# Optimization experiments

Hardware: AMD Instinct MI355X
Metric: run time of the kernel (lower is better)

Reference implementation:

```python
import jax, jax.numpy as jnp
import numpy as np

NEG_INF = jnp.finfo(jnp.float32).min


def _continual_mask(attach_test_after, Q, K, test_num, chunk_size):
    """Boolean allowed-mask [B, 1, Q, K] replicating get_continual_mask +
    the per-batch test-query/train-key override in forward()."""
    k_train = K - test_num * chunk_size
    q_train = Q - test_num * chunk_size
    qi = jnp.arange(Q)[:, None]          # [Q,1]
    kj = jnp.arange(K)[None, :]          # [1,K]
    # base causal mask with diagonal offset K-Q (train queries)
    base = kj <= qi + (K - Q)            # [Q,K]
    # block-diagonal tril for test-query / test-key region
    dq = qi - q_train                    # local test row (negative for train rows, unused there)
    dk = kj - k_train
    block = (kj >= k_train) & (dk <= dq) & ((dk // chunk_size) == (dq // chunk_size))
    # per-batch: test query in chunk n may see train keys <= attach_test_after[b, n]
    chunk_idx = jnp.clip(dq[:, 0], 0, None) // chunk_size          # [Q]
    att = attach_test_after[:, chunk_idx]                          # [B,Q]
    train_key_allowed = kj[None, :, :] <= att[:, :, None]          # [B,Q,K]
    allowed = jnp.where(qi < q_train, base[None],
                        jnp.where(kj[None] < k_train, train_key_allowed, block[None]))
    return allowed[:, None]              # [B,1,Q,K]


def setup_inputs() -> dict:
    key = jax.random.key(0)
    k1, k2, k3, k4 = jax.random.split(key, 4)
    B, L, H, D = 4, 2048, 8, 64
    test_num, train_len = 64, 1536
    return {
        "queries": jax.random.normal(k1, (B, L, H, D), dtype=jnp.float32),
        "keys": jax.random.normal(k2, (B, L, H, D), dtype=jnp.float32),
        "values": jax.random.normal(k3, (B, L, H, D), dtype=jnp.float32),
        "attach_test_after": jax.random.randint(k4, (B, test_num), 0, train_len).astype(jnp.int64),
        "train_len": train_len,
    }


def reference(queries, keys, values, attach_test_after, train_len):
    B, Lq, H, Dqk = queries.shape
    test_num = attach_test_after.shape[1]
    chunk_size = (Lq - train_len) // test_num
    q = jnp.transpose(queries, (0, 2, 1, 3))   # [B,H,Lq,D]
    k = jnp.transpose(keys, (0, 2, 1, 3))      # [B,H,Lk,D]
    v = jnp.transpose(values, (0, 2, 1, 3))    # [B,H,Lk,Dv]
    Lk = k.shape[2]
    # vanilla path: scaled QK^T + continual mask + softmax + AV
    logits = jnp.einsum('bhmd,bhnd->bhmn', q, k) / jnp.sqrt(jnp.float32(Dqk))
    allowed = _continual_mask(attach_test_after, Lq, Lk, test_num, chunk_size)
    logits = jnp.where(allowed, logits, NEG_INF)
    attn = jax.nn.softmax(logits, axis=-1)
    out = jnp.einsum('bhmn,bhnd->bhmd', attn, v)
    return out.transpose(0, 2, 1, 3).reshape(B, Lq, H * v.shape[-1])  # b l (h d)
```

## Files before the change

kernel.cpp:

```cpp
#include <hip/hip_runtime.h>
#include <hip/hip_bf16.h>

typedef __bf16 bf16_t;
typedef __bf16 bf16x8 __attribute__((ext_vector_type(8)));
typedef float  f32x4  __attribute__((ext_vector_type(4)));

#define MFMA16(a, b, c) __builtin_amdgcn_mfma_f32_16x16x32_bf16((a), (b), (c), 0, 0, 0)

constexpr int Bc = 4, Lc = 2048, Hc = 8, Dc = 64;
constexpr int HD = Hc * Dc;
constexpr int TRAINc = 1536;
constexpr int KT = 64;
constexpr int PST = 64;
constexpr float QSCALE = 0.125f * 1.4426950408889634f;

__global__ void prep_k(const float* __restrict__ K, bf16_t* __restrict__ Kb) {
  size_t g = ((size_t)blockIdx.x * 256 + threadIdx.x) * 8;
  float4 a = *(const float4*)(K + g);
  float4 b = *(const float4*)(K + g + 4);
  bf16x8 v;
  v[0] = (bf16_t)a.x; v[1] = (bf16_t)a.y; v[2] = (bf16_t)a.z; v[3] = (bf16_t)a.w;
  v[4] = (bf16_t)b.x; v[5] = (bf16_t)b.y; v[6] = (bf16_t)b.z; v[7] = (bf16_t)b.w;
  *(bf16x8*)(Kb + g) = v;
}

__global__ void prep_v(const float* __restrict__ V, bf16_t* __restrict__ Vt) {
  __shared__ bf16_t T[64][72];
  const int bid = blockIdx.x;
  const int kt = bid & 31, h = (bid >> 5) & 7, b = bid >> 8;
  const int t = (int)threadIdx.x;
  {
    int kl = t >> 2, dp = (t & 3) << 4;
    const float* s = V + ((size_t)(b * Lc + kt * 64 + kl) * Hc + h) * Dc + dp;
    bf16x8 v0, v1;
    float4 f;
    f = *(const float4*)(s);      v0[0]=(bf16_t)f.x; v0[1]=(bf16_t)f.y; v0[2]=(bf16_t)f.z; v0[3]=(bf16_t)f.w;
    f = *(const float4*)(s + 4);  v0[4]=(bf16_t)f.x; v0[5]=(bf16_t)f.y; v0[6]=(bf16_t)f.z; v0[7]=(bf16_t)f.w;
    f = *(const float4*)(s + 8);  v1[0]=(bf16_t)f.x; v1[1]=(bf16_t)f.y; v1[2]=(bf16_t)f.z; v1[3]=(bf16_t)f.w;
    f = *(const float4*)(s + 12); v1[4]=(bf16_t)f.x; v1[5]=(bf16_t)f.y; v1[6]=(bf16_t)f.z; v1[7]=(bf16_t)f.w;
    *(bf16x8*)&T[kl][dp] = v0;
    *(bf16x8*)&T[kl][dp + 8] = v1;
  }
  __syncthreads();
  {
    int d = t >> 2, kp = (t & 3) << 4;
    bf16x8 o0, o1;
#pragma unroll
    for (int i = 0; i < 8; ++i) { o0[i] = T[kp + i][d]; o1[i] = T[kp + 8 + i][d]; }
    bf16_t* dst = Vt + ((size_t)((b * Hc + h) * Dc + d)) * Lc + kt * 64 + kp;
    *(bf16x8*)dst = o0;
    *(bf16x8*)(dst + 8) = o1;
  }
}

static __device__ __forceinline__ void load16(const bf16_t* g, bf16_t* l) {
  __builtin_amdgcn_global_load_lds(
      (const __attribute__((address_space(1))) unsigned int*)g,
      (__attribute__((address_space(3))) unsigned int*)l, 16, 0, 0);
}

__global__ __launch_bounds__(256, 4)
void continual_attn(const float* __restrict__ Qg, const bf16_t* __restrict__ Kb,
                    const bf16_t* __restrict__ Vt, const int* __restrict__ ATT,
                    float* __restrict__ OUT)
{
  __shared__ __align__(16) bf16_t Klds[2][KT * 64];
  __shared__ __align__(16) bf16_t Vlds[2][Dc * KT];
  __shared__ __align__(16) bf16_t Plds[4][16 * PST];

  const int bid  = blockIdx.x;
  const int qblk = 31 - (bid >> 5);
  const int h    = bid & 7;
  const int b    = (bid >> 3) & 3;
  const int q0   = qblk * 64;

  const int tid  = (int)threadIdx.x;
  const int wave = tid >> 6;
  const int lane = tid & 63;
  const int quad = lane >> 4;
  const int col  = lane & 15;
  const int qw   = q0 + wave * 16;

  const bool testblk = (q0 >= TRAINc);
  int kend[4], cstart[4], qir[4];
#pragma unroll
  for (int r = 0; r < 4; ++r) {
    int qi = qw + quad * 4 + r;
    qir[r] = qi;
    if (testblk) {
      kend[r]   = ATT[b * 64 + ((qi - TRAINc) >> 3)] + 1;
      cstart[r] = qi & ~7;
    } else {
      kend[r]   = qi + 1;
      cstart[r] = 0;
    }
  }

  int ntA, ndiag, kfull_end;
  if (testblk) {
    int c0 = (q0 - TRAINc) >> 3;
    int amax = 0;
#pragma unroll
    for (int i = 0; i < 8; ++i) {
      int a = ATT[b * 64 + c0 + i];
      amax = (a > amax) ? a : amax;
    }
    int w0 = (qw - TRAINc) >> 3;
    int a0 = ATT[b * 64 + w0], a1 = ATT[b * 64 + w0 + 1];
    kfull_end = ((a0 < a1) ? a0 : a1) + 1;
    ntA = (amax >> 6) + 1;
    ndiag = 1;
  } else {
    ntA = qblk + 1;
    ndiag = 0;
    kfull_end = qw + 1;
  }
  const int ntot = ntA + ndiag;

  const size_t bhQ = (size_t)b * Lc * HD + (size_t)h * Dc;

  const int kr = tid >> 3;
  const bf16_t* ksrcA = Kb + bhQ + (size_t)kr * HD + (((tid & 7) ^ (kr & 7)) << 3);
  const bf16_t* vsrcA = Vt + ((size_t)((b * Hc + h) * Dc + kr)) * Lc + (((tid & 7) ^ (kr & 7)) << 3);
  const bf16_t* vsrcB = vsrcA + (size_t)32 * Lc;

  bf16x8 aq[2];
  {
    const float* qp = Qg + bhQ + (size_t)(qw + col) * HD + quad * 8;
#pragma unroll
    for (int t = 0; t < 2; ++t) {
      float4 lo = *(const float4*)(qp + t * 32);
      float4 hi = *(const float4*)(qp + t * 32 + 4);
      bf16x8 v;
      v[0] = (bf16_t)(lo.x * QSCALE); v[1] = (bf16_t)(lo.y * QSCALE);
      v[2] = (bf16_t)(lo.z * QSCALE); v[3] = (bf16_t)(lo.w * QSCALE);
      v[4] = (bf16_t)(hi.x * QSCALE); v[5] = (bf16_t)(hi.y * QSCALE);
      v[6] = (bf16_t)(hi.z * QSCALE); v[7] = (bf16_t)(hi.w * QSCALE);
      aq[t] = v;
    }
  }

  float lsumL[4] = {0.f, 0.f, 0.f, 0.f};
  f32x4 o[4] = {{0,0,0,0},{0,0,0,0},{0,0,0,0},{0,0,0,0}};
  const int cA = ((quad ^ (col & 7)) << 3);

  load16(ksrcA, Klds[0] + wave * 512);
  load16(ksrcA + (size_t)32 * HD, Klds[0] + 2048 + wave * 512);
  load16(vsrcA, Vlds[0] + wave * 512);
  load16(vsrcB, Vlds[0] + 2048 + wave * 512);

  for (int ti = 0; ti < ntot; ++ti) {
    const int buf = ti & 1;
    __syncthreads();

    if (ti + 1 < ntot) {
      const int kn = (ti + 1 < ntA) ? (ti + 1) * KT : q0;
      load16(ksrcA + (size_t)kn * HD, Klds[1 - buf] + wave * 512);
      load16(ksrcA + (size_t)(kn + 32) * HD, Klds[1 - buf] + 2048 + wave * 512);
      load16(vsrcA + kn, Vlds[1 - buf] + wave * 512);
      load16(vsrcB + kn, Vlds[1 - buf] + 2048 + wave * 512);
    }

    const bf16_t* kb = Klds[buf];
    const bf16_t* vbuf = Vlds[buf];
    const int k0 = (ti < ntA) ? ti * KT : q0;

    f32x4 sf[4] = {{0,0,0,0},{0,0,0,0},{0,0,0,0},{0,0,0,0}};
#pragma unroll
    for (int kg = 0; kg < 4; ++kg) {
      const bf16_t* krow = kb + (kg * 16 + col) * 64;
      bf16x8 k0f = *(const bf16x8*)(krow + cA);
      bf16x8 k1f = *(const bf16x8*)(krow + (cA ^ 32));
      sf[kg] = MFMA16(aq[0], k0f, sf[kg]);
      sf[kg] = MFMA16(aq[1], k1f, sf[kg]);
    }

    const int mode = (ti >= ntA) ? 2 : ((k0 + KT <= kfull_end) ? 0 : 1);
    if (mode == 1) {
#pragma unroll
      for (int kg = 0; kg < 4; ++kg) {
        const int kgv = k0 + kg * 16 + col;
#pragma unroll
        for (int r = 0; r < 4; ++r)
          if (kgv >= kend[r]) sf[kg][r] = -1e30f;
      }
    } else if (mode == 2) {
#pragma unroll
      for (int kg = 0; kg < 4; ++kg) {
        const int kgv = k0 + kg * 16 + col;
#pragma unroll
        for (int r = 0; r < 4; ++r)
          if (kgv < cstart[r] || kgv > qir[r]) sf[kg][r] = -1e30f;
      }
    }

    bf16_t* pw = Plds[wave];
#pragma unroll
    for (int kg = 0; kg < 4; ++kg) {
#pragma unroll
      for (int r = 0; r < 4; ++r) {
        float p = __builtin_amdgcn_exp2f(sf[kg][r]);
        lsumL[r] += p;
        const int row = quad * 4 + r;
        pw[row * PST + (((kg * 2 + (col >> 3)) ^ (row & 7)) << 3) + (col & 7)] = (bf16_t)p;
      }
    }
    bf16x8 pa0 = *(const bf16x8*)&pw[col * PST + cA];
    bf16x8 pa1 = *(const bf16x8*)&pw[col * PST + (cA ^ 32)];

#pragma unroll
    for (int t = 0; t < 4; ++t) {
      const bf16_t* vrow = vbuf + (t * 16 + col) * 64;
      bf16x8 v0 = *(const bf16x8*)(vrow + cA);
      bf16x8 v1 = *(const bf16x8*)(vrow + (cA ^ 32));
      o[t] = MFMA16(pa0, v0, o[t]);
      o[t] = MFMA16(pa1, v1, o[t]);
    }
  }

#pragma unroll
  for (int r = 0; r < 4; ++r) {
    float rs = lsumL[r];
    rs += __shfl_xor(rs, 1);
    rs += __shfl_xor(rs, 2);
    rs += __shfl_xor(rs, 4);
    rs += __shfl_xor(rs, 8);
    float inv = 1.f / rs;
    int qi = qw + quad * 4 + r;
    float* op = OUT + ((size_t)b * Lc + qi) * HD + (size_t)h * Dc + col;
    op[0]  = o[0][r] * inv;
    op[16] = o[1][r] * inv;
    op[32] = o[2][r] * inv;
    op[48] = o[3][r] * inv;
  }
}

extern "C" void kernel_launch(void* const* d_in, const int* in_sizes, int n_in,
                              void* d_out, int out_size, void* d_ws, size_t ws_size,
                              hipStream_t stream) {
  const float* Q   = (const float*)d_in[0];
  const float* K   = (const float*)d_in[1];
  const float* V   = (const float*)d_in[2];
  const int*   ATT = (const int*)d_in[3];
  float* OUT = (float*)d_out;
  (void)in_sizes; (void)n_in; (void)out_size; (void)ws_size;

  const size_t NE = (size_t)Bc * Lc * Hc * Dc;
  bf16_t* Kb = (bf16_t*)d_ws;
  bf16_t* Vt = Kb + NE;

  prep_k<<<dim3((unsigned)(NE / 8 / 256)), dim3(256), 0, stream>>>(K, Kb);
  prep_v<<<dim3(Bc * Hc * (Lc / 64)), dim3(256), 0, stream>>>(V, Vt);
  continual_attn<<<dim3(Bc * Hc * 32), dim3(256), 0, stream>>>(Q, Kb, Vt, ATT, OUT);
}
```

Baseline: 131.6 us.

## Use two-wave blocks with 32 query rows per wave and merge K/V prep kernels

The attention kernel moves from 4 waves handling 16 query rows each to 2 waves handling 32 rows each. Every K and V fragment read from LDS now feeds MFMAs for two row blocks, which halves LDS traffic per unit of compute. The K and V conversion kernels are also merged into a single launch to save one kernel launch. In exchange each wave needs more registers, and each block has fewer waves to hide latency, with a launch bound of 2 blocks per SIMD group.

```diff
diff --git a/kernel.cpp b/kernel.cpp
--- a/kernel.cpp
+++ b/kernel.cpp
@@ -10,25 +10,25 @@
 constexpr int Bc = 4, Lc = 2048, Hc = 8, Dc = 64;
 constexpr int HD = Hc * Dc;
 constexpr int TRAINc = 1536;
-constexpr int KT = 64;
-constexpr int PST = 64;
 constexpr float QSCALE = 0.125f * 1.4426950408889634f;
 
-__global__ void prep_k(const float* __restrict__ K, bf16_t* __restrict__ Kb) {
-  size_t g = ((size_t)blockIdx.x * 256 + threadIdx.x) * 8;
-  float4 a = *(const float4*)(K + g);
-  float4 b = *(const float4*)(K + g + 4);
-  bf16x8 v;
-  v[0] = (bf16_t)a.x; v[1] = (bf16_t)a.y; v[2] = (bf16_t)a.z; v[3] = (bf16_t)a.w;
-  v[4] = (bf16_t)b.x; v[5] = (bf16_t)b.y; v[6] = (bf16_t)b.z; v[7] = (bf16_t)b.w;
-  *(bf16x8*)(Kb + g) = v;
-}
-
-__global__ void prep_v(const float* __restrict__ V, bf16_t* __restrict__ Vt) {
+__global__ void prep_kv(const float* __restrict__ K, const float* __restrict__ V,
+                        bf16_t* __restrict__ Kb, bf16_t* __restrict__ Vt) {
   __shared__ bf16_t T[64][72];
-  const int bid = blockIdx.x;
+  const int bid0 = blockIdx.x;
+  const int t = (int)threadIdx.x;
+  if (bid0 < 2048) {
+    size_t g = ((size_t)bid0 * 256 + t) * 8;
+    float4 a = *(const float4*)(K + g);
+    float4 b = *(const float4*)(K + g + 4);
+    bf16x8 v;
+    v[0] = (bf16_t)a.x; v[1] = (bf16_t)a.y; v[2] = (bf16_t)a.z; v[3] = (bf16_t)a.w;
+    v[4] = (bf16_t)b.x; v[5] = (bf16_t)b.y; v[6] = (bf16_t)b.z; v[7] = (bf16_t)b.w;
+    *(bf16x8*)(Kb + g) = v;
+    return;
+  }
+  const int bid = bid0 - 2048;
   const int kt = bid & 31, h = (bid >> 5) & 7, b = bid >> 8;
-  const int t = (int)threadIdx.x;
   {
     int kl = t >> 2, dp = (t & 3) << 4;
     const float* s = V + ((size_t)(b * Lc + kt * 64 + kl) * Hc + h) * Dc + dp;
@@ -59,14 +59,14 @@
       (__attribute__((address_space(3))) unsigned int*)l, 16, 0, 0);
 }
 
-__global__ __launch_bounds__(256, 4)
+__global__ __launch_bounds__(128, 2)
 void continual_attn(const float* __restrict__ Qg, const bf16_t* __restrict__ Kb,
                     const bf16_t* __restrict__ Vt, const int* __restrict__ ATT,
                     float* __restrict__ OUT)
 {
-  __shared__ __align__(16) bf16_t Klds[2][KT * 64];
-  __shared__ __align__(16) bf16_t Vlds[2][Dc * KT];
-  __shared__ __align__(16) bf16_t Plds[4][16 * PST];
+  __shared__ __align__(16) bf16_t Klds[2][64 * 64];
+  __shared__ __align__(16) bf16_t Vlds[2][64 * 64];
+  __shared__ __align__(16) bf16_t Plds[2][32 * 64];
 
   const int bid  = blockIdx.x;
   const int qblk = 31 - (bid >> 5);
@@ -79,24 +79,27 @@
   const int lane = tid & 63;
   const int quad = lane >> 4;
   const int col  = lane & 15;
-  const int qw   = q0 + wave * 16;
+  const int qw   = q0 + wave * 32;
 
   const bool testblk = (q0 >= TRAINc);
-  int kend[4], cstart[4], qir[4];
-#pragma unroll
-  for (int r = 0; r < 4; ++r) {
-    int qi = qw + quad * 4 + r;
-    qir[r] = qi;
-    if (testblk) {
-      kend[r]   = ATT[b * 64 + ((qi - TRAINc) >> 3)] + 1;
-      cstart[r] = qi & ~7;
-    } else {
-      kend[r]   = qi + 1;
-      cstart[r] = 0;
-    }
-  }
-
-  int ntA, ndiag, kfull_end;
+  int kend[2][4], cstart[2][4], qir[2][4];
+#pragma unroll
+  for (int rb = 0; rb < 2; ++rb) {
+#pragma unroll
+    for (int r = 0; r < 4; ++r) {
+      int qi = qw + rb * 16 + quad * 4 + r;
+      qir[rb][r] = qi;
+      if (testblk) {
+        kend[rb][r]   = ATT[b * 64 + ((qi - TRAINc) >> 3)] + 1;
+        cstart[rb][r] = qi & ~7;
+      } else {
+        kend[rb][r]   = qi + 1;
+        cstart[rb][r] = 0;
+      }
+    }
+  }
+
+  int ntA, ntot, kfull_end;
   if (testblk) {
     int c0 = (q0 - TRAINc) >> 3;
     int amax = 0;
@@ -106,27 +109,32 @@
       amax = (a > amax) ? a : amax;
     }
     int w0 = (qw - TRAINc) >> 3;
-    int a0 = ATT[b * 64 + w0], a1 = ATT[b * 64 + w0 + 1];
-    kfull_end = ((a0 < a1) ? a0 : a1) + 1;
+    int amin = 0x7fffffff;
+#pragma unroll
+    for (int i = 0; i < 4; ++i) {
+      int a = ATT[b * 64 + w0 + i];
+      amin = (a < amin) ? a : amin;
+    }
+    kfull_end = amin + 1;
     ntA = (amax >> 6) + 1;
-    ndiag = 1;
+    ntot = ntA + 1;
   } else {
     ntA = qblk + 1;
-    ndiag = 0;
+    ntot = ntA;
     kfull_end = qw + 1;
   }
-  const int ntot = ntA + ndiag;
 
   const size_t bhQ = (size_t)b * Lc * HD + (size_t)h * Dc;
 
   const int kr = tid >> 3;
-  const bf16_t* ksrcA = Kb + bhQ + (size_t)kr * HD + (((tid & 7) ^ (kr & 7)) << 3);
-  const bf16_t* vsrcA = Vt + ((size_t)((b * Hc + h) * Dc + kr)) * Lc + (((tid & 7) ^ (kr & 7)) << 3);
-  const bf16_t* vsrcB = vsrcA + (size_t)32 * Lc;
-
-  bf16x8 aq[2];
-  {
-    const float* qp = Qg + bhQ + (size_t)(qw + col) * HD + quad * 8;
+  const int sl = ((tid & 7) ^ (kr & 7)) << 3;
+  const bf16_t* ksrc0 = Kb + bhQ + (size_t)kr * HD + sl;
+  const bf16_t* vsrc0 = Vt + ((size_t)((b * Hc + h) * Dc + kr)) * Lc + sl;
+
+  bf16x8 aq[2][2];
+#pragma unroll
+  for (int rb = 0; rb < 2; ++rb) {
+    const float* qp = Qg + bhQ + (size_t)(qw + rb * 16 + col) * HD + quad * 8;
 #pragma unroll
     for (int t = 0; t < 2; ++t) {
       float4 lo = *(const float4*)(qp + t * 32);
@@ -136,102 +144,126 @@
       v[2] = (bf16_t)(lo.z * QSCALE); v[3] = (bf16_t)(lo.w * QSCALE);
       v[4] = (bf16_t)(hi.x * QSCALE); v[5] = (bf16_t)(hi.y * QSCALE);
       v[6] = (bf16_t)(hi.z * QSCALE); v[7] = (bf16_t)(hi.w * QSCALE);
-      aq[t] = v;
-    }
-  }
-
-  float lsumL[4] = {0.f, 0.f, 0.f, 0.f};
-  f32x4 o[4] = {{0,0,0,0},{0,0,0,0},{0,0,0,0},{0,0,0,0}};
+      aq[rb][t] = v;
+    }
+  }
+
+  float lsumL[2][4] = {{0.f,0.f,0.f,0.f},{0.f,0.f,0.f,0.f}};
+  f32x4 o[2][4] = {};
   const int cA = ((quad ^ (col & 7)) << 3);
 
-  load16(ksrcA, Klds[0] + wave * 512);
-  load16(ksrcA + (size_t)32 * HD, Klds[0] + 2048 + wave * 512);
-  load16(vsrcA, Vlds[0] + wave * 512);
-  load16(vsrcB, Vlds[0] + 2048 + wave * 512);
+#pragma unroll
+  for (int c = 0; c < 4; ++c) {
+    load16(ksrc0 + (size_t)(16 * c) * HD, Klds[0] + wave * 512 + c * 1024);
+    load16(vsrc0 + (size_t)(16 * c) * Lc, Vlds[0] + wave * 512 + c * 1024);
+  }
 
   for (int ti = 0; ti < ntot; ++ti) {
     const int buf = ti & 1;
     __syncthreads();
 
     if (ti + 1 < ntot) {
-      const int kn = (ti + 1 < ntA) ? (ti + 1) * KT : q0;
-      load16(ksrcA + (size_t)kn * HD, Klds[1 - buf] + wave * 512);
-      load16(ksrcA + (size_t)(kn + 32) * HD, Klds[1 - buf] + 2048 + wave * 512);
-      load16(vsrcA + kn, Vlds[1 - buf] + wave * 512);
-      load16(vsrcB + kn, Vlds[1 - buf] + 2048 + wave * 512);
+      const int kn = (ti + 1 < ntA) ? (ti + 1) * 64 : q0;
+      bf16_t* kd = Klds[1 - buf] + wave * 512;
+      bf16_t* vd = Vlds[1 - buf] + wave * 512;
+#pragma unroll
+      for (int c = 0; c < 4; ++c) {
+        load16(ksrc0 + (size_t)(kn + 16 * c) * HD, kd + c * 1024);
+        load16(vsrc0 + (size_t)(16 * c) * Lc + kn, vd + c * 1024);
+      }
     }
 
     const bf16_t* kb = Klds[buf];
-    const bf16_t* vbuf = Vlds[buf];
-    const int k0 = (ti < ntA) ? ti * KT : q0;
-
-    f32x4 sf[4] = {{0,0,0,0},{0,0,0,0},{0,0,0,0},{0,0,0,0}};
+    const bf16_t* vb = Vlds[buf];
+    const int k0 = (ti < ntA) ? ti * 64 : q0;
+
+    f32x4 sf[2][4] = {};
 #pragma unroll
     for (int kg = 0; kg < 4; ++kg) {
       const bf16_t* krow = kb + (kg * 16 + col) * 64;
       bf16x8 k0f = *(const bf16x8*)(krow + cA);
       bf16x8 k1f = *(const bf16x8*)(krow + (cA ^ 32));
-      sf[kg] = MFMA16(aq[0], k0f, sf[kg]);
-      sf[kg] = MFMA16(aq[1], k1f, sf[kg]);
-    }
-
-    const int mode = (ti >= ntA) ? 2 : ((k0 + KT <= kfull_end) ? 0 : 1);
+#pragma unroll
+      for (int rb = 0; rb < 2; ++rb) {
+        sf[rb][kg] = MFMA16(aq[rb][0], k0f, sf[rb][kg]);
+        sf[rb][kg] = MFMA16(aq[rb][1], k1f, sf[rb][kg]);
+      }
+    }
+
+    const int mode = (testblk && ti >= ntA) ? 2 : ((k0 + 64 <= kfull_end) ? 0 : 1);
     if (mode == 1) {
 #pragma unroll
       for (int kg = 0; kg < 4; ++kg) {
         const int kgv = k0 + kg * 16 + col;
 #pragma unroll
-        for (int r = 0; r < 4; ++r)
-          if (kgv >= kend[r]) sf[kg][r] = -1e30f;
+        for (int rb = 0; rb < 2; ++rb)
+#pragma unroll
+          for (int r = 0; r < 4; ++r)
+            if (kgv >= kend[rb][r]) sf[rb][kg][r] = -1e30f;
       }
     } else if (mode == 2) {
 #pragma unroll
       for (int kg = 0; kg < 4; ++kg) {
         const int kgv = k0 + kg * 16 + col;
 #pragma unroll
-        for (int r = 0; r < 4; ++r)
-          if (kgv < cstart[r] || kgv > qir[r]) sf[kg][r] = -1e30f;
+        for (int rb = 0; rb < 2; ++rb)
+#pragma unroll
+          for (int r = 0; r < 4; ++r)
+            if (kgv < cstart[rb][r] || kgv > qir[rb][r]) sf[rb][kg][r] = -1e30f;
       }
     }
 
     bf16_t* pw = Plds[wave];
 #pragma unroll
-    for (int kg = 0; kg < 4; ++kg) {
-#pragma unroll
-      for (int r = 0; r < 4; ++r) {
-        float p = __builtin_amdgcn_exp2f(sf[kg][r]);
-        lsumL[r] += p;
-        const int row = quad * 4 + r;
-        pw[row * PST + (((kg * 2 + (col >> 3)) ^ (row & 7)) << 3) + (col & 7)] = (bf16_t)p;
-      }
-    }
-    bf16x8 pa0 = *(const bf16x8*)&pw[col * PST + cA];
-    bf16x8 pa1 = *(const bf16x8*)&pw[col * PST + (cA ^ 32)];
+    for (int rb = 0; rb < 2; ++rb) {
+#pragma unroll
+      for (int kg = 0; kg < 4; ++kg) {
+#pragma unroll
+        for (int r = 0; r < 4; ++r) {
+          float p = __builtin_amdgcn_exp2f(sf[rb][kg][r]);
+          lsumL[rb][r] += p;
+          const int row = rb * 16 + quad * 4 + r;
+          pw[row * 64 + (((kg * 2 + (col >> 3)) ^ (row & 7)) << 3) + (col & 7)] = (bf16_t)p;
+        }
+      }
+    }
+    bf16x8 pa[2][2];
+#pragma unroll
+    for (int rb = 0; rb < 2; ++rb) {
+      pa[rb][0] = *(const bf16x8*)&pw[(rb * 16 + col) * 64 + cA];
+      pa[rb][1] = *(const bf16x8*)&pw[(rb * 16 + col) * 64 + (cA ^ 32)];
+    }
 
 #pragma unroll
     for (int t = 0; t < 4; ++t) {
-      const bf16_t* vrow = vbuf + (t * 16 + col) * 64;
+      const bf16_t* vrow = vb + (t * 16 + col) * 64;
       bf16x8 v0 = *(const bf16x8*)(vrow + cA);
       bf16x8 v1 = *(const bf16x8*)(vrow + (cA ^ 32));
-      o[t] = MFMA16(pa0, v0, o[t]);
-      o[t] = MFMA16(pa1, v1, o[t]);
-    }
-  }
-
-#pragma unroll
-  for (int r = 0; r < 4; ++r) {
-    float rs = lsumL[r];
-    rs += __shfl_xor(rs, 1);
-    rs += __shfl_xor(rs, 2);
-    rs += __shfl_xor(rs, 4);
-    rs += __shfl_xor(rs, 8);
-    float inv = 1.f / rs;
-    int qi = qw + quad * 4 + r;
-    float* op = OUT + ((size_t)b * Lc + qi) * HD + (size_t)h * Dc + col;
-    op[0]  = o[0][r] * inv;
-    op[16] = o[1][r] * inv;
-    op[32] = o[2][r] * inv;
-    op[48] = o[3][r] * inv;
+#pragma unroll
+      for (int rb = 0; rb < 2; ++rb) {
+        o[rb][t] = MFMA16(pa[rb][0], v0, o[rb][t]);
+        o[rb][t] = MFMA16(pa[rb][1], v1, o[rb][t]);
+      }
+    }
+  }
+
+#pragma unroll
+  for (int rb = 0; rb < 2; ++rb) {
+#pragma unroll
+    for (int r = 0; r < 4; ++r) {
+      float rs = lsumL[rb][r];
+      rs += __shfl_xor(rs, 1);
+      rs += __shfl_xor(rs, 2);
+      rs += __shfl_xor(rs, 4);
+      rs += __shfl_xor(rs, 8);
+      float inv = 1.f / rs;
+      int qi = qw + rb * 16 + quad * 4 + r;
+      float* op = OUT + ((size_t)b * Lc + qi) * HD + (size_t)h * Dc + col;
+      op[0]  = o[rb][0][r] * inv;
+      op[16] = o[rb][1][r] * inv;
+      op[32] = o[rb][2][r] * inv;
+      op[48] = o[rb][3][r] * inv;
+    }
   }
 }
 
@@ -249,7 +281,6 @@
   bf16_t* Kb = (bf16_t*)d_ws;
   bf16_t* Vt = Kb + NE;
 
-  prep_k<<<dim3((unsigned)(NE / 8 / 256)), dim3(256), 0, stream>>>(K, Kb);
-  prep_v<<<dim3(Bc * Hc * (Lc / 64)), dim3(256), 0, stream>>>(V, Vt);
-  continual_attn<<<dim3(Bc * Hc * 32), dim3(256), 0, stream>>>(Q, Kb, Vt, ATT, OUT);
-}
+  prep_kv<<<dim3(2048 + 1024), dim3(256), 0, stream>>>(K, V, Kb, Vt);
+  continual_attn<<<dim3(Bc * Hc * 32), dim3(128), 0, stream>>>(Q, Kb, Vt, ATT, OUT);
+}
```

Result: slower. 139.9 us (+6.3%).
